# Kernel optimization log

Hardware: AMD Instinct MI355X
Metric: run time of the kernel (lower is better)

The kernel has to match this reference:

```python
import jax, jax.numpy as jnp
import numpy as np
from jax import lax

E = 300      # _embsize
H = 32       # attention heads
ADIM = 64    # projection_dim (attention and values dim)
FF = 100     # feedforward hidden dim
NK = 11      # gaussian kernels
NCONV = 5    # conv kernel sizes 1..5
COUT = 16    # conv out channels for k>=2

def _kernel_mus(n):
    l = [1.0]
    b = 2.0 / (n - 1)
    l.append(1 - b / 2)
    for i in range(1, n - 1):
        l.append(l[i] - b)
    return l

def _kernel_sigmas(n):
    b = 2.0 / (n - 1)
    return [0.0001] + [0.5 * b] * (n - 1)

MU = jnp.asarray(_kernel_mus(NK), jnp.float32).reshape(1, 1, 1, 1, NK)
SIG = jnp.asarray(_kernel_sigmas(NK), jnp.float32).reshape(1, 1, 1, 1, NK)

def _pos_features(T, d):
    # allennlp add_positional_features, min_timescale=1, max_timescale=1e4, d even
    nt = d // 2
    inv = np.exp(np.arange(nt, dtype=np.float32) * -(np.log(1e4) / (nt - 1)))
    pos = np.arange(T, dtype=np.float32)[:, None] * inv[None, :]
    return jnp.asarray(np.concatenate([np.sin(pos), np.cos(pos)], axis=1))

def _layer_norm(x, g, b, eps=1e-6):
    m = jnp.mean(x, -1, keepdims=True)
    s = jnp.std(x, -1, keepdims=True)  # biased std, as allennlp LayerNorm
    return g * (x - m) / (s + eps) + b

def _mhsa(x, mask, Wc, bc, Wo, bo):
    # allennlp MultiHeadSelfAttention: combined projection, scale=sqrt(input_dim//heads)
    B, T, _ = x.shape
    comb = x @ Wc + bc                                   # [B,T,3*ADIM]
    q, k, v = comb[..., :ADIM], comb[..., ADIM:2 * ADIM], comb[..., 2 * ADIM:]
    dh = ADIM // H
    split = lambda t: t.reshape(B, T, H, dh).transpose(0, 2, 1, 3)
    q, k, v = split(q), split(k), split(v)
    scale = float(np.sqrt(E // H))
    sim = jnp.einsum('bhqd,bhkd->bhqk', q / scale, k)
    m = mask[:, None, None, :]
    p = jax.nn.softmax(sim * m, axis=-1) * m             # old allennlp masked_softmax
    p = p / (jnp.sum(p, -1, keepdims=True) + 1e-13)
    o = jnp.einsum('bhqk,bhkd->bhqd', p, v).transpose(0, 2, 1, 3).reshape(B, T, ADIM)
    return o @ Wo + bo

def _encode(x, mask, W1, b1, W2, b2, ffg, ffb, Wc, bc, Wo, bo, lng, lnb):
    # StackedSelfAttentionEncoder, 1 layer, all dropouts = 0
    out = x + _pos_features(x.shape[1], E)[None]
    ff = jax.nn.relu(out @ W1 + b1) @ W2 + b2
    ff = _layer_norm(ff + out, ffg, ffb)                 # residual (dims match)
    att = _mhsa(ff, mask, Wc, bc, Wo, bo)
    return _layer_norm(att + ff, lng, lnb)

def _conv(x, w, b, k):
    if k > 1:
        x = jnp.pad(x, ((0, 0), (0, 0), (0, k - 1), (0, k - 1)))  # ConstantPad2d(0,k-1,0,k-1)
    y = lax.conv_general_dilated(x, w, (1, 1), 'VALID',
                                 dimension_numbers=('NCHW', 'OIHW', 'NCHW'))
    y = y + b[None, :, None, None]
    if k > 1:
        y = jnp.max(y, axis=1, keepdims=True)            # MaxPool3d over channel dim
    return y

def setup_inputs() -> dict:
    key = jax.random.key(0)
    ks = iter(jax.random.split(key, 40))
    B, Q, D = 16, 32, 512
    nrm = lambda shape, s=0.05: jax.random.normal(next(ks), shape, jnp.float32) * s
    return {
        'query_embeddings': jax.random.normal(next(ks), (B, Q, E), jnp.float32),
        'document_embeddings': jax.random.normal(next(ks), (B, D, E), jnp.float32),
        'query_pad_oov_mask': jnp.ones((B, Q), jnp.float32),
        'document_pad_oov_mask': jnp.ones((B, D), jnp.float32),
        'query_idfs': jax.random.uniform(next(ks), (B, Q, 1), jnp.float32),
        'document_idfs': jax.random.uniform(next(ks), (B, D, 1), jnp.float32),
        'W1': nrm((E, FF)), 'b1': jnp.zeros((FF,), jnp.float32),
        'W2': nrm((FF, E)), 'b2': jnp.zeros((E,), jnp.float32),
        'ffg': jnp.ones((E,), jnp.float32), 'ffb': jnp.zeros((E,), jnp.float32),
        'Wc': nrm((E, 3 * ADIM)), 'bc': jnp.zeros((3 * ADIM,), jnp.float32),
        'Wo': nrm((ADIM, E)), 'bo': jnp.zeros((E,), jnp.float32),
        'lng': jnp.ones((E,), jnp.float32), 'lnb': jnp.zeros((E,), jnp.float32),
        'c1w': nrm((1, 2, 1, 1)), 'c1b': jnp.zeros((1,), jnp.float32),
        'c2w': nrm((COUT, 2, 2, 2)), 'c2b': jnp.zeros((COUT,), jnp.float32),
        'c3w': nrm((COUT, 2, 3, 3)), 'c3b': jnp.zeros((COUT,), jnp.float32),
        'c4w': nrm((COUT, 2, 4, 4)), 'c4b': jnp.zeros((COUT,), jnp.float32),
        'c5w': nrm((COUT, 2, 5, 5)), 'c5b': jnp.zeros((COUT,), jnp.float32),
        'dw': nrm((1, NK * NCONV)), 'db': jnp.zeros((1,), jnp.float32),
        'dmw': nrm((1, NK * NCONV)), 'dmb': jnp.zeros((1,), jnp.float32),
        'cw': nrm((1, 2)),
    }

def reference(query_embeddings, document_embeddings, query_pad_oov_mask,
              document_pad_oov_mask, query_idfs, document_idfs,
              W1, b1, W2, b2, ffg, ffb, Wc, bc, Wo, bo, lng, lnb,
              c1w, c1b, c2w, c2b, c3w, c3b, c4w, c4b, c5w, c5b,
              dw, db, dmw, dmb, cw):
    qm, dmask = query_pad_oov_mask, document_pad_oov_mask
    enc = lambda x, m: _encode(x, m, W1, b1, W2, b2, ffg, ffb, Wc, bc, Wo, bo, lng, lnb)
    q_ctx = enc(query_embeddings, qm) * qm[..., None]
    d_ctx = enc(document_embeddings, dmask) * dmask[..., None]
    # cosine on raw embeddings, dot product on contextualized
    qn = query_embeddings / (jnp.linalg.norm(query_embeddings, axis=-1, keepdims=True) + 1e-13)
    dn = document_embeddings / (jnp.linalg.norm(document_embeddings, axis=-1, keepdims=True) + 1e-13)
    cos = jnp.einsum('bqe,bde->bqd', qn, dn)[:, None]
    dot = jnp.einsum('bqe,bde->bqd', q_ctx, d_ctx)[:, None]
    combined = jnp.tanh(jnp.concatenate([cos, dot], axis=1))     # [B,2,Q,D]
    convs = [_conv(combined, w, b, k) for k, (w, b) in enumerate(
        [(c1w, c1b), (c2w, c2b), (c3w, c3b), (c4w, c4b), (c5w, c5b)], start=1)]
    all_conv = jnp.concatenate(convs, axis=1)[..., None]         # [B,5,Q,D,1]
    qd_mask = (qm[:, :, None] * dmask[:, None, :])[:, None, :, :, None]  # [B,1,Q,D,1]
    raw = jnp.exp(-(all_conv - MU) ** 2 / (2.0 * SIG ** 2))      # [B,5,Q,D,NK]
    masked = raw * qd_mask
    doc_len = jnp.sum(dmask, 1)                                  # [B]
    pkq = jnp.sum(masked, axis=3)                                # [B,5,Q,NK]
    log_pkq = jnp.log(jnp.clip(pkq, 1e-10, None)) * qm[:, None, :, None]
    per_kernel = jnp.sum(log_pkq, axis=2)                        # [B,5,NK]
    pkq_mean = pkq / doc_len[:, None, None, None]
    log_pkq_mean = jnp.log(jnp.clip(pkq_mean, 1e-10, None)) * qm[:, None, :, None]
    per_kernel_mean = jnp.sum(log_pkq_mean, axis=2)
    B = per_kernel.shape[0]
    d1 = per_kernel.reshape(B, -1) @ dw.T + db
    d2 = per_kernel_mean.reshape(B, -1) @ dmw.T + dmb
    return (jnp.concatenate([d1, d2], axis=1) @ cw.T)[:, 0]
```

## Files before the change

kernel.cpp:

```cpp
#include <hip/hip_runtime.h>

namespace {

constexpr int E_  = 300;
constexpr int FF_ = 100;
constexpr int AD_ = 64;
constexpr int NH_ = 32;
constexpr int CD_ = 192;
constexpr int B_  = 16;
constexpr int TQ_ = 32;
constexpr int TD_ = 512;
constexpr int NK_ = 11;
constexpr int DOCBLK_ = 512;

__device__ __forceinline__ float wave_sum(float v) {
#pragma unroll
  for (int o = 32; o > 0; o >>= 1) v += __shfl_down(v, o);
  return v;
}

__device__ __forceinline__ int swz16(int e, int t) {
  return e * 16 + (t ^ (((e >> 2) & 7) << 1));
}

__device__ __forceinline__ void fma4(float4& a, float s, const float4& w) {
  a.x = fmaf(s, w.x, a.x); a.y = fmaf(s, w.y, a.y);
  a.z = fmaf(s, w.z, a.z); a.w = fmaf(s, w.w, a.w);
}

__global__ __launch_bounds__(256)
void encode_front_v4(const float* __restrict__ qe, const float* __restrict__ de,
                     const float* __restrict__ W1, const float* __restrict__ b1,
                     const float* __restrict__ W2, const float* __restrict__ b2,
                     const float* __restrict__ ffg, const float* __restrict__ ffb,
                     const float* __restrict__ Wc, const float* __restrict__ bc,
                     float* __restrict__ ffq, float* __restrict__ combq,
                     float* __restrict__ qn,
                     float* __restrict__ ffd, float* __restrict__ combd,
                     float* __restrict__ dnT)
{
  __shared__ float  s_A[4800];
  __shared__ float  s_h1[1600];
  __shared__ float4 s_w4[1500];
  __shared__ float  s_stat[16][17];
  __shared__ float  s_norm[16];

  const int tid = threadIdx.x;
  const int ct = tid & 31, tg = tid >> 5;
  const int t0 = tg * 2;
  const bool doc = (blockIdx.x < DOCBLK_);
  const int sb = doc ? blockIdx.x : (blockIdx.x - DOCBLK_);
  const float* xs = (doc ? de : qe) + (size_t)sb * 16 * E_;
  float* ffo = doc ? ffd : ffq;
  float* cmo = doc ? combd : combq;
  const size_t tok0 = (size_t)sb * 16;
  const int bb_ = doc ? (int)(tok0 >> 9) : (int)(tok0 >> 5);
  const int tp0 = doc ? (int)(tok0 & 511) : (int)(tok0 & 31);

  for (int i = tid; i < 1200; i += 256) {
    const float4 v = *(const float4*)(xs + (size_t)i * 4);
    const int t = i / 75, e0 = (i % 75) * 4;
    s_A[swz16(e0 + 0, t)] = v.x; s_A[swz16(e0 + 1, t)] = v.y;
    s_A[swz16(e0 + 2, t)] = v.z; s_A[swz16(e0 + 3, t)] = v.w;
  }
  __syncthreads();
  {
    const int tk = tid & 15, ch = tid >> 4;
    const int kb = ch * 19, ke = (kb + 19 < 300) ? kb + 19 : 300;
    float ss = 0.f;
    for (int k = kb; k < ke; ++k) { const float v = s_A[swz16(k, tk)]; ss = fmaf(v, v, ss); }
    s_stat[ch][tk] = ss;
  }
  __syncthreads();
  if (tid < 16) {
    float s = 0.f;
#pragma unroll
    for (int i = 0; i < 16; ++i) s += s_stat[i][tid];
    s_norm[tid] = 1.f / (sqrtf(s) + 1e-13f);
  }
  __syncthreads();
  for (int i = tid; i < 1200; i += 256) {
    const int t = i / 75, e0 = (i % 75) * 4;
    const int tp = tp0 + t;
    const float nm = s_norm[t];
#pragma unroll
    for (int j = 0; j < 4; ++j) {
      const int e = e0 + j;
      const int slot = swz16(e, t);
      const float raw = s_A[slot];
      if (doc) dnT[((size_t)bb_ * E_ + e) * 512 + tp] = raw * nm;
      else     qn[(tok0 + t) * E_ + e] = raw * nm;
      const int f = (e < 150) ? e : e - 150;
      const float ang = __expf(-0.061814365f * (float)f) * (float)tp;
      s_A[slot] = raw + ((e < 150) ? sinf(ang) : cosf(ang));
    }
  }
  __syncthreads();

  {
    const int cq = (ct < 25) ? ct : 24;
    float4 a1[2];
    a1[0] = make_float4(0.f, 0.f, 0.f, 0.f);
    a1[1] = make_float4(0.f, 0.f, 0.f, 0.f);
    for (int k0 = 0; k0 < 300; k0 += 60) {
      for (int i = tid; i < 1500; i += 256)
        s_w4[i] = *(const float4*)(W1 + (size_t)k0 * FF_ + (size_t)i * 4);
      __syncthreads();
#pragma unroll 6
      for (int kk = 0; kk < 60; ++kk) {
        const float2 xv = *(const float2*)&s_A[swz16(k0 + kk, t0)];
        const float4 w = s_w4[kk * 25 + cq];
        fma4(a1[0], xv.x, w); fma4(a1[1], xv.y, w);
      }
      __syncthreads();
    }
    if (ct < 25) {
      const float4 bb = *(const float4*)&b1[4 * ct];
#pragma unroll
      for (int r = 0; r < 2; ++r) {
        const int t = t0 + r;
        const float4 a = (r == 0) ? a1[0] : a1[1];
        s_h1[swz16(4 * ct + 0, t)] = fmaxf(a.x + bb.x, 0.f);
        s_h1[swz16(4 * ct + 1, t)] = fmaxf(a.y + bb.y, 0.f);
        s_h1[swz16(4 * ct + 2, t)] = fmaxf(a.z + bb.z, 0.f);
        s_h1[swz16(4 * ct + 3, t)] = fmaxf(a.w + bb.w, 0.f);
      }
    }
    __syncthreads();
  }

  {
    const int q2 = (ct < 11) ? ct + 64 : 74;
    const bool val2 = (ct < 11);
    float4 a2[3][2];
#pragma unroll
    for (int p = 0; p < 3; ++p)
#pragma unroll
      for (int r = 0; r < 2; ++r) a2[p][r] = make_float4(0.f, 0.f, 0.f, 0.f);
    for (int k0 = 0; k0 < 100; k0 += 20) {
      for (int i = tid; i < 1500; i += 256)
        s_w4[i] = *(const float4*)(W2 + (size_t)k0 * E_ + (size_t)i * 4);
      __syncthreads();
#pragma unroll 5
      for (int kk = 0; kk < 20; ++kk) {
        const float2 hv = *(const float2*)&s_h1[swz16(k0 + kk, t0)];
        const float4 w0 = s_w4[kk * 75 + ct];
        const float4 w1 = s_w4[kk * 75 + ct + 32];
        const float4 w2 = s_w4[kk * 75 + q2];
        fma4(a2[0][0], hv.x, w0); fma4(a2[0][1], hv.y, w0);
        fma4(a2[1][0], hv.x, w1); fma4(a2[1][1], hv.y, w1);
        fma4(a2[2][0], hv.x, w2); fma4(a2[2][1], hv.y, w2);
      }
      __syncthreads();
    }
    float sum[2] = {0.f, 0.f}, sq[2] = {0.f, 0.f};
#pragma unroll
    for (int p = 0; p < 3; ++p) {
      const int qq = (p == 0) ? ct : (p == 1) ? ct + 32 : q2;
      const float4 bb = *(const float4*)&b2[4 * qq];
      const bool ok = (p < 2) || val2;
#pragma unroll
      for (int r = 0; r < 2; ++r) {
        const int t = t0 + r;
        float4 v = a2[p][r];
        v.x += bb.x + s_A[swz16(4 * qq + 0, t)];
        v.y += bb.y + s_A[swz16(4 * qq + 1, t)];
        v.z += bb.z + s_A[swz16(4 * qq + 2, t)];
        v.w += bb.w + s_A[swz16(4 * qq + 3, t)];
        a2[p][r] = v;
        if (ok) {
          sum[r] += v.x + v.y + v.z + v.w;
          sq[r] = fmaf(v.x, v.x, fmaf(v.y, v.y, fmaf(v.z, v.z, fmaf(v.w, v.w, sq[r]))));
        }
      }
    }
#pragma unroll
    for (int m = 1; m <= 16; m <<= 1) {
#pragma unroll
      for (int r = 0; r < 2; ++r) {
        sum[r] += __shfl_xor(sum[r], m);
        sq[r]  += __shfl_xor(sq[r], m);
      }
    }
    float mean[2], rstd[2];
#pragma unroll
    for (int r = 0; r < 2; ++r) {
      mean[r] = sum[r] * (1.f / 300.f);
      const float var = fmaxf(sq[r] * (1.f / 300.f) - mean[r] * mean[r], 0.f);
      rstd[r] = 1.f / (sqrtf(var) + 1e-6f);
    }
    __syncthreads();
#pragma unroll
    for (int p = 0; p < 3; ++p) {
      if (p == 2 && !val2) break;
      const int qq = (p == 0) ? ct : (p == 1) ? ct + 32 : q2;
      const int c0 = 4 * qq;
      const float4 g4 = *(const float4*)&ffg[c0];
      const float4 b4 = *(const float4*)&ffb[c0];
#pragma unroll
      for (int r = 0; r < 2; ++r) {
        const int t = t0 + r;
        const float4 v = a2[p][r];
        float4 fv;
        fv.x = fmaf(g4.x, (v.x - mean[r]) * rstd[r], b4.x);
        fv.y = fmaf(g4.y, (v.y - mean[r]) * rstd[r], b4.y);
        fv.z = fmaf(g4.z, (v.z - mean[r]) * rstd[r], b4.z);
        fv.w = fmaf(g4.w, (v.w - mean[r]) * rstd[r], b4.w);
        *(float4*)&ffo[(tok0 + t) * E_ + c0] = fv;
        s_A[swz16(c0 + 0, t)] = fv.x; s_A[swz16(c0 + 1, t)] = fv.y;
        s_A[swz16(c0 + 2, t)] = fv.z; s_A[swz16(c0 + 3, t)] = fv.w;
      }
    }
    __syncthreads();
  }

  {
    const int q3 = (ct < 16) ? ct + 32 : 47;
    float4 a3[2][2];
#pragma unroll
    for (int p = 0; p < 2; ++p)
#pragma unroll
      for (int r = 0; r < 2; ++r) a3[p][r] = make_float4(0.f, 0.f, 0.f, 0.f);
    for (int k0 = 0; k0 < 300; k0 += 30) {
      for (int i = tid; i < 1440; i += 256)
        s_w4[i] = *(const float4*)(Wc + (size_t)k0 * CD_ + (size_t)i * 4);
      __syncthreads();
#pragma unroll 6
      for (int kk = 0; kk < 30; ++kk) {
        const float2 xv = *(const float2*)&s_A[swz16(k0 + kk, t0)];
        const float4 w0 = s_w4[kk * 48 + ct];
        const float4 w1 = s_w4[kk * 48 + q3];
        fma4(a3[0][0], xv.x, w0); fma4(a3[0][1], xv.y, w0);
        fma4(a3[1][0], xv.x, w1); fma4(a3[1][1], xv.y, w1);
      }
      __syncthreads();
    }
    const float4 bb0 = *(const float4*)&bc[4 * ct];
#pragma unroll
    for (int r = 0; r < 2; ++r) {
      float4 o = a3[0][r];
      o.x += bb0.x; o.y += bb0.y; o.z += bb0.z; o.w += bb0.w;
      *(float4*)&cmo[(tok0 + t0 + r) * CD_ + 4 * ct] = o;
    }
    if (ct < 16) {
      const float4 bb1 = *(const float4*)&bc[4 * (ct + 32)];
#pragma unroll
      for (int r = 0; r < 2; ++r) {
        float4 o = a3[1][r];
        o.x += bb1.x; o.y += bb1.y; o.z += bb1.z; o.w += bb1.w;
        *(float4*)&cmo[(tok0 + t0 + r) * CD_ + 4 * (ct + 32)] = o;
      }
    }
  }
}

template <int T>
__global__ __launch_bounds__(512)
void attn(const float* __restrict__ comb, const float* __restrict__ mask,
          float* __restrict__ o)
{
  __shared__ float4 s_kv[T];
  __shared__ float  s_m[T];
  const int bh = blockIdx.x, b = bh / NH_, h = bh % NH_;
  const int tid = threadIdx.x;
  const float* cb = comb + (size_t)b * T * CD_;
  if (tid < T) {
    const float* c = cb + (size_t)tid * CD_;
    const float m = mask[b * T + tid];
    s_kv[tid] = make_float4(c[AD_ + 2 * h] * m, c[AD_ + 2 * h + 1] * m,
                            c[2 * AD_ + 2 * h], c[2 * AD_ + 2 * h + 1]);
    s_m[tid] = m;
  }
  __syncthreads();
  if (tid < T) {
    const float* c = cb + (size_t)tid * CD_;
    const float q0 = c[2 * h] * (1.f / 3.f);
    const float q1 = c[2 * h + 1] * (1.f / 3.f);
    float M = -1e30f;
    for (int j = 0; j < T; ++j) {
      const float4 kv = s_kv[j];
      M = fmaxf(M, fmaf(q0, kv.x, q1 * kv.y));
    }
    float S = 0.f, W = 0.f, a0 = 0.f, a1 = 0.f;
    for (int j = 0; j < T; ++j) {
      const float4 kv = s_kv[j];
      const float s = fmaf(q0, kv.x, q1 * kv.y);
      const float z = __expf(s - M);
      const float w = z * s_m[j];
      S += z; W += w;
      a0 = fmaf(w, kv.z, a0);
      a1 = fmaf(w, kv.w, a1);
    }
    const float dn = 1.f / (W + 1e-13f * S);
    float* op = o + (size_t)(b * T + tid) * AD_ + 2 * h;
    op[0] = a0 * dn;
    op[1] = a1 * dn;
  }
}

__global__ __launch_bounds__(256)
void encode_back_v2(const float* __restrict__ oq, const float* __restrict__ od,
                    const float* __restrict__ ffq, const float* __restrict__ ffd,
                    const float* __restrict__ Wo, const float* __restrict__ bo,
                    const float* __restrict__ lng, const float* __restrict__ lnb,
                    const float* __restrict__ qm, const float* __restrict__ dm,
                    float* __restrict__ qctx, float* __restrict__ dctxT)
{
  __shared__ float  s_O[1024];
  __shared__ float4 s_w4[1200];

  const int tid = threadIdx.x;
  const int ct = tid & 31, tg = tid >> 5;
  const int t0 = tg * 2;
  const bool doc = (blockIdx.x < DOCBLK_);
  const int sb = doc ? blockIdx.x : (blockIdx.x - DOCBLK_);
  const size_t tok0 = (size_t)sb * 16;
  const float* op = doc ? od : oq;
  const float* ffp = doc ? ffd : ffq;
  const float* mp = doc ? dm : qm;
  const int bb_ = doc ? (int)(tok0 >> 9) : 0;
  const int tp0 = doc ? (int)(tok0 & 511) : 0;

  {
    const int i = tid;
    const int t = i >> 4, c0 = (i & 15) * 4;
    const float4 v = *(const float4*)(op + (tok0 + t) * AD_ + c0);
    s_O[swz16(c0 + 0, t)] = v.x; s_O[swz16(c0 + 1, t)] = v.y;
    s_O[swz16(c0 + 2, t)] = v.z; s_O[swz16(c0 + 3, t)] = v.w;
  }
  __syncthreads();

  const int q2 = (ct < 11) ? ct + 64 : 74;
  const bool val2 = (ct < 11);
  float4 a[3][2];
#pragma unroll
  for (int p = 0; p < 3; ++p)
#pragma unroll
    for (int r = 0; r < 2; ++r) a[p][r] = make_float4(0.f, 0.f, 0.f, 0.f);
  for (int k0 = 0; k0 < 64; k0 += 16) {
    for (int i = tid; i < 1200; i += 256)
      s_w4[i] = *(const float4*)(Wo + (size_t)k0 * E_ + (size_t)i * 4);
    __syncthreads();
#pragma unroll 4
    for (int kk = 0; kk < 16; ++kk) {
      const float2 ov = *(const float2*)&s_O[swz16(k0 + kk, t0)];
      const float4 w0 = s_w4[kk * 75 + ct];
      const float4 w1 = s_w4[kk * 75 + ct + 32];
      const float4 w2 = s_w4[kk * 75 + q2];
      fma4(a[0][0], ov.x, w0); fma4(a[0][1], ov.y, w0);
      fma4(a[1][0], ov.x, w1); fma4(a[1][1], ov.y, w1);
      fma4(a[2][0], ov.x, w2); fma4(a[2][1], ov.y, w2);
    }
    __syncthreads();
  }
  float sum[2] = {0.f, 0.f}, sq[2] = {0.f, 0.f};
#pragma unroll
  for (int p = 0; p < 3; ++p) {
    const int qq = (p == 0) ? ct : (p == 1) ? ct + 32 : q2;
    const float4 bb = *(const float4*)&bo[4 * qq];
    const bool ok = (p < 2) || val2;
#pragma unroll
    for (int r = 0; r < 2; ++r) {
      const int t = t0 + r;
      const float4 f4 = *(const float4*)(ffp + (tok0 + t) * E_ + 4 * qq);
      float4 v = a[p][r];
      v.x += bb.x + f4.x; v.y += bb.y + f4.y;
      v.z += bb.z + f4.z; v.w += bb.w + f4.w;
      a[p][r] = v;
      if (ok) {
        sum[r] += v.x + v.y + v.z + v.w;
        sq[r] = fmaf(v.x, v.x, fmaf(v.y, v.y, fmaf(v.z, v.z, fmaf(v.w, v.w, sq[r]))));
      }
    }
  }
#pragma unroll
  for (int m = 1; m <= 16; m <<= 1) {
#pragma unroll
    for (int r = 0; r < 2; ++r) {
      sum[r] += __shfl_xor(sum[r], m);
      sq[r]  += __shfl_xor(sq[r], m);
    }
  }
#pragma unroll
  for (int r = 0; r < 2; ++r) {
    const int t = t0 + r;
    const float mean = sum[r] * (1.f / 300.f);
    const float var  = fmaxf(sq[r] * (1.f / 300.f) - mean * mean, 0.f);
    const float rstd = 1.f / (sqrtf(var) + 1e-6f);
    const float mk = mp[tok0 + t];
#pragma unroll
    for (int p = 0; p < 3; ++p) {
      if (p == 2 && !val2) break;
      const int qq = (p == 0) ? ct : (p == 1) ? ct + 32 : q2;
      const int c0 = 4 * qq;
      const float4 g4 = *(const float4*)&lng[c0];
      const float4 b4 = *(const float4*)&lnb[c0];
      const float4 v = a[p][r];
      float4 fv;
      fv.x = fmaf(g4.x, (v.x - mean) * rstd, b4.x) * mk;
      fv.y = fmaf(g4.y, (v.y - mean) * rstd, b4.y) * mk;
      fv.z = fmaf(g4.z, (v.z - mean) * rstd, b4.z) * mk;
      fv.w = fmaf(g4.w, (v.w - mean) * rstd, b4.w) * mk;
      if (doc) {
        const int tp = tp0 + t;
        dctxT[((size_t)bb_ * E_ + c0 + 0) * 512 + tp] = fv.x;
        dctxT[((size_t)bb_ * E_ + c0 + 1) * 512 + tp] = fv.y;
        dctxT[((size_t)bb_ * E_ + c0 + 2) * 512 + tp] = fv.z;
        dctxT[((size_t)bb_ * E_ + c0 + 3) * 512 + tp] = fv.w;
      } else {
        *(float4*)&qctx[(tok0 + t) * E_ + c0] = fv;
      }
    }
  }
}

__global__ __launch_bounds__(512)
void simtanh_v2(const float* __restrict__ qctx, const float* __restrict__ qn,
                const float* __restrict__ dctxT, const float* __restrict__ dnT,
                float* __restrict__ combined)
{
  __shared__ float s_q[2 * 16 * 304];
  __shared__ float s_part[8 * 32 * 64];

  const int bid = blockIdx.x;
  const int sub = bid & 15, b = bid >> 4;
  const int qh = sub >> 3, dc = sub & 7;
  const int tid = threadIdx.x;
  const int ep = tid >> 6, dlane = tid & 63;
  const int d = dc * 64 + dlane;

  const float* qc  = qctx + ((size_t)b * 32 + qh * 16) * E_;
  const float* qnp = qn   + ((size_t)b * 32 + qh * 16) * E_;
  for (int i = tid; i < 1200; i += 512) {
    const int q = i / 75, e0 = (i % 75) * 4;
    *(float4*)&s_q[(0 * 16 + q) * 304 + e0] = *(const float4*)(qc + q * E_ + e0);
    *(float4*)&s_q[(1 * 16 + q) * 304 + e0] = *(const float4*)(qnp + q * E_ + e0);
  }
  __syncthreads();

  const float* dct = dctxT + (size_t)b * E_ * 512 + d;
  const float* dnt = dnT   + (size_t)b * E_ * 512 + d;
  float accD[16], accC[16];
#pragma unroll
  for (int q = 0; q < 16; ++q) { accD[q] = 0.f; accC[q] = 0.f; }
  const int es = ep * 40, ee = (es + 40 < 300) ? es + 40 : 300;
  for (int e0 = es; e0 < ee; e0 += 4) {
    const float dv0 = dct[(size_t)(e0 + 0) * 512];
    const float dv1 = dct[(size_t)(e0 + 1) * 512];
    const float dv2 = dct[(size_t)(e0 + 2) * 512];
    const float dv3 = dct[(size_t)(e0 + 3) * 512];
    const float dn0 = dnt[(size_t)(e0 + 0) * 512];
    const float dn1 = dnt[(size_t)(e0 + 1) * 512];
    const float dn2 = dnt[(size_t)(e0 + 2) * 512];
    const float dn3 = dnt[(size_t)(e0 + 3) * 512];
#pragma unroll
    for (int q = 0; q < 16; ++q) {
      const float4 qd = *(const float4*)&s_q[(0 * 16 + q) * 304 + e0];
      const float4 qc4 = *(const float4*)&s_q[(1 * 16 + q) * 304 + e0];
      float aD = accD[q], aC = accC[q];
      aD = fmaf(qd.x, dv0, aD); aD = fmaf(qd.y, dv1, aD);
      aD = fmaf(qd.z, dv2, aD); aD = fmaf(qd.w, dv3, aD);
      aC = fmaf(qc4.x, dn0, aC); aC = fmaf(qc4.y, dn1, aC);
      aC = fmaf(qc4.z, dn2, aC); aC = fmaf(qc4.w, dn3, aC);
      accD[q] = aD; accC[q] = aC;
    }
  }
#pragma unroll
  for (int q = 0; q < 16; ++q) {
    s_part[(ep * 32 + q * 2 + 0) * 64 + dlane] = accC[q];
    s_part[(ep * 32 + q * 2 + 1) * 64 + dlane] = accD[q];
  }
  __syncthreads();
  const int s0 = (tid >> 6) * 4;
#pragma unroll
  for (int si = 0; si < 4; ++si) {
    const int s = s0 + si;
    float v = 0.f;
#pragma unroll
    for (int p = 0; p < 8; ++p) v += s_part[(p * 32 + s) * 64 + dlane];
    const int q = s >> 1, typ = s & 1;
    combined[(((size_t)b * 2 + typ) * 32 + qh * 16 + q) * 512 + d] = tanhf(v);
  }
}

template <int K>
__device__ __forceinline__ float conv_max16(const float* __restrict__ s_in, int j,
                                            const float* __restrict__ w,
                                            const float* __restrict__ bias)
{
  float patch[2][K][K];
#pragma unroll
  for (int c = 0; c < 2; ++c)
#pragma unroll
    for (int di = 0; di < K; ++di)
#pragma unroll
      for (int dj = 0; dj < K; ++dj)
        patch[c][di][dj] = s_in[(c * 5 + di) * 516 + j + dj];
  float best = -1e30f;
#pragma unroll
  for (int oc = 0; oc < 16; ++oc) {
    float acc = bias[oc];
#pragma unroll
    for (int c = 0; c < 2; ++c)
#pragma unroll
      for (int di = 0; di < K; ++di)
#pragma unroll
        for (int dj = 0; dj < K; ++dj)
          acc = fmaf(patch[c][di][dj], w[((oc * 2 + c) * K + di) * K + dj], acc);
    best = fmaxf(best, acc);
  }
  return best;
}

__global__ __launch_bounds__(512)
void conv_all(const float* __restrict__ combined,
              const float* __restrict__ c1w, const float* __restrict__ c1b,
              const float* __restrict__ c2w, const float* __restrict__ c2b,
              const float* __restrict__ c3w, const float* __restrict__ c3b,
              const float* __restrict__ c4w, const float* __restrict__ c4b,
              const float* __restrict__ c5w, const float* __restrict__ c5b,
              float* __restrict__ convout)
{
  __shared__ float s_in[2 * 5 * 516];
  __shared__ float s_w[1730];
  __shared__ float s_b[66];
  const int blk = blockIdx.x, b = blk >> 5, i = blk & 31;
  const int tid = threadIdx.x;
  for (int idx = tid; idx < 2 * 5 * 516; idx += 512) {
    const int c = idx / (5 * 516), rem = idx % (5 * 516), r = rem / 516, j = rem % 516;
    const int row = i + r;
    float v = 0.f;
    if (row < 32 && j < 512)
      v = combined[((size_t)(b * 2 + c) * 32 + row) * 512 + j];
    s_in[idx] = v;
  }
  if (tid < 2)   s_w[tid] = c1w[tid];
  if (tid < 128) s_w[2 + tid] = c2w[tid];
  if (tid < 288) s_w[130 + tid] = c3w[tid];
  s_w[418 + tid] = c4w[tid];
  for (int idx = tid; idx < 800; idx += 512) s_w[930 + idx] = c5w[idx];
  if (tid == 0) s_b[0] = c1b[0];
  if (tid < 16) {
    s_b[1 + tid]  = c2b[tid];
    s_b[17 + tid] = c3b[tid];
    s_b[33 + tid] = c4b[tid];
    s_b[49 + tid] = c5b[tid];
  }
  __syncthreads();
  const int j = tid;
  const float o1 = fmaf(s_in[j], s_w[0], fmaf(s_in[5 * 516 + j], s_w[1], s_b[0]));
  convout[((size_t)(b * 5 + 0) * 32 + i) * 512 + j] = o1;
  convout[((size_t)(b * 5 + 1) * 32 + i) * 512 + j] = conv_max16<2>(s_in, j, s_w + 2,   s_b + 1);
  convout[((size_t)(b * 5 + 2) * 32 + i) * 512 + j] = conv_max16<3>(s_in, j, s_w + 130, s_b + 17);
  convout[((size_t)(b * 5 + 3) * 32 + i) * 512 + j] = conv_max16<4>(s_in, j, s_w + 418, s_b + 33);
  convout[((size_t)(b * 5 + 4) * 32 + i) * 512 + j] = conv_max16<5>(s_in, j, s_w + 930, s_b + 49);
}

__global__ __launch_bounds__(512)
void rbf_pkq(const float* __restrict__ convout, const float* __restrict__ dmask,
             const float* __restrict__ qmask, float* __restrict__ pkq)
{
  __shared__ float red[8][NK_];
  const int id = blockIdx.x;
  const int q = id & 31;
  const int b = id / 160;
  const int tid = threadIdx.x;
  const float x = convout[(size_t)id * 512 + tid];
  const float dmv = dmask[b * 512 + tid];
  const float mu[NK_]  = {1.f, .9f, .7f, .5f, .3f, .1f, -.1f, -.3f, -.5f, -.7f, -.9f};
  const float nis[NK_] = {-5e7f, -50.f, -50.f, -50.f, -50.f, -50.f,
                          -50.f, -50.f, -50.f, -50.f, -50.f};
  const int lane = tid & 63, w = tid >> 6;
#pragma unroll
  for (int k = 0; k < NK_; ++k) {
    const float df = x - mu[k];
    float v = __expf(df * df * nis[k]) * dmv;
    v = wave_sum(v);
    if (lane == 0) red[w][k] = v;
  }
  __syncthreads();
  if (tid < NK_) {
    float s = 0.f;
#pragma unroll
    for (int ww = 0; ww < 8; ++ww) s += red[ww][tid];
    pkq[(size_t)id * NK_ + tid] = s * qmask[b * 32 + q];
  }
}

__global__ __launch_bounds__(64)
void final_k(const float* __restrict__ pkq, const float* __restrict__ qmask,
             const float* __restrict__ dmask,
             const float* __restrict__ dw, const float* __restrict__ db,
             const float* __restrict__ dmw, const float* __restrict__ dmb,
             const float* __restrict__ cw, float* __restrict__ out)
{
  const int b = blockIdx.x, tid = threadIdx.x;
  float dl = 0.f;
  for (int j = tid; j < 512; j += 64) dl += dmask[b * 512 + j];
  dl = wave_sum(dl);
  dl = __shfl(dl, 0);
  float v1 = 0.f, v2 = 0.f;
  if (tid < 55) {
    const int c = tid / NK_, k = tid % NK_;
    const float rdl = 1.f / dl;
    float s1 = 0.f, s2 = 0.f;
    for (int q = 0; q < 32; ++q) {
      const float p = pkq[(size_t)((b * 5 + c) * 32 + q) * NK_ + k];
      const float qmv = qmask[b * 32 + q];
      s1 += logf(fmaxf(p, 1e-10f)) * qmv;
      s2 += logf(fmaxf(p * rdl, 1e-10f)) * qmv;
    }
    v1 = s1 * dw[tid];
    v2 = s2 * dmw[tid];
  }
  v1 = wave_sum(v1);
  v2 = wave_sum(v2);
  if (tid == 0) out[b] = (v1 + db[0]) * cw[0] + (v2 + dmb[0]) * cw[1];
}

}

extern "C" void kernel_launch(void* const* d_in, const int* in_sizes, int n_in,
                              void* d_out, int out_size, void* d_ws, size_t ws_size,
                              hipStream_t stream)
{
  const float* qe  = (const float*)d_in[0];
  const float* de  = (const float*)d_in[1];
  const float* qm  = (const float*)d_in[2];
  const float* dm  = (const float*)d_in[3];
  const float* W1  = (const float*)d_in[6];
  const float* b1  = (const float*)d_in[7];
  const float* W2  = (const float*)d_in[8];
  const float* b2  = (const float*)d_in[9];
  const float* ffg = (const float*)d_in[10];
  const float* ffb = (const float*)d_in[11];
  const float* Wc  = (const float*)d_in[12];
  const float* bc  = (const float*)d_in[13];
  const float* Wo  = (const float*)d_in[14];
  const float* bo  = (const float*)d_in[15];
  const float* lng = (const float*)d_in[16];
  const float* lnb = (const float*)d_in[17];
  const float* c1w = (const float*)d_in[18];
  const float* c1b = (const float*)d_in[19];
  const float* c2w = (const float*)d_in[20];
  const float* c2b = (const float*)d_in[21];
  const float* c3w = (const float*)d_in[22];
  const float* c3b = (const float*)d_in[23];
  const float* c4w = (const float*)d_in[24];
  const float* c4b = (const float*)d_in[25];
  const float* c5w = (const float*)d_in[26];
  const float* c5b = (const float*)d_in[27];
  const float* dwp  = (const float*)d_in[28];
  const float* dbp  = (const float*)d_in[29];
  const float* dmwp = (const float*)d_in[30];
  const float* dmbp = (const float*)d_in[31];
  const float* cwp  = (const float*)d_in[32];

  float* ws = (float*)d_ws;
  size_t off = 0;
  auto alloc = [&](size_t n) { float* p = ws + off; off += n; return p; };
  float* ffq      = alloc((size_t)B_ * TQ_ * E_);
  float* combq    = alloc((size_t)B_ * TQ_ * CD_);
  float* oq       = alloc((size_t)B_ * TQ_ * AD_);
  float* qctx     = alloc((size_t)B_ * TQ_ * E_);
  float* qn       = alloc((size_t)B_ * TQ_ * E_);
  float* ffd      = alloc((size_t)B_ * TD_ * E_);
  float* combd    = alloc((size_t)B_ * TD_ * CD_);
  float* od       = alloc((size_t)B_ * TD_ * AD_);
  float* dctxT    = alloc((size_t)B_ * E_ * TD_);
  float* dnT      = alloc((size_t)B_ * E_ * TD_);
  float* combined = alloc((size_t)B_ * 2 * TQ_ * TD_);
  float* convout  = alloc((size_t)B_ * 5 * TQ_ * TD_);
  float* pkq      = alloc((size_t)B_ * 5 * TQ_ * NK_);

  encode_front_v4<<<DOCBLK_ + 32, 256, 0, stream>>>(
      qe, de, W1, b1, W2, b2, ffg, ffb, Wc, bc,
      ffq, combq, qn, ffd, combd, dnT);
  attn<TQ_><<<B_ * NH_, 64, 0, stream>>>(combq, qm, oq);
  attn<TD_><<<B_ * NH_, 512, 0, stream>>>(combd, dm, od);
  encode_back_v2<<<DOCBLK_ + 32, 256, 0, stream>>>(
      oq, od, ffq, ffd, Wo, bo, lng, lnb, qm, dm, qctx, dctxT);
  simtanh_v2<<<256, 512, 0, stream>>>(qctx, qn, dctxT, dnT, combined);
  conv_all<<<B_ * 32, 512, 0, stream>>>(
      combined, c1w, c1b, c2w, c2b, c3w, c3b, c4w, c4b, c5w, c5b, convout);
  rbf_pkq<<<B_ * 5 * TQ_, 512, 0, stream>>>(convout, dm, qm, pkq);
  final_k<<<B_, 64, 0, stream>>>(pkq, qm, dm, dwp, dbp, dmwp, dmbp, cwp,
                                 (float*)d_out);
}
```

Before: 377.2 us.

## Double-buffer weight tiles with async global-to-LDS loads in encoder kernels

Weight chunks for the W1, W2, Wc and Wo matmuls in the front and back encoder kernels are now staged with `__builtin_amdgcn_global_load_lds` into a two-slot LDS buffer. The next chunk, including the first chunk of the following matmul, is fetched while the current one is computed, which removes one barrier per chunk and the register round-trip of the staging copy. The bias, residual and layer-norm epilogues are folded into the last chunk iteration, and padded lanes skip work early. The cost is doubled weight LDS, which may lower occupancy, and correctness depends on the barriers waiting for the async loads to finish.

```diff
diff --git a/kernel.cpp b/kernel.cpp
--- a/kernel.cpp
+++ b/kernel.cpp
@@ -28,8 +28,20 @@
   a.z = fmaf(s, w.z, a.z); a.w = fmaf(s, w.w, a.w);
 }
 
+__device__ __forceinline__ void gl_lds16(const float4* g, float4* l) {
+  __builtin_amdgcn_global_load_lds(
+      (const __attribute__((address_space(1))) void*)g,
+      (__attribute__((address_space(3))) void*)l, 16, 0, 0);
+}
+
+__device__ __forceinline__ void stage_chunk(const float4* __restrict__ src,
+                                            float4* __restrict__ dst,
+                                            int n, int tid) {
+  for (int j = tid; j < n; j += 256) gl_lds16(src + j, dst + j);
+}
+
 __global__ __launch_bounds__(256)
-void encode_front_v4(const float* __restrict__ qe, const float* __restrict__ de,
+void encode_front_v5(const float* __restrict__ qe, const float* __restrict__ de,
                      const float* __restrict__ W1, const float* __restrict__ b1,
                      const float* __restrict__ W2, const float* __restrict__ b2,
                      const float* __restrict__ ffg, const float* __restrict__ ffb,
@@ -41,7 +53,7 @@
 {
   __shared__ float  s_A[4800];
   __shared__ float  s_h1[1600];
-  __shared__ float4 s_w4[1500];
+  __shared__ float4 s_w[2][1500];
   __shared__ float  s_stat[16][17];
   __shared__ float  s_norm[16];
 
@@ -57,6 +69,12 @@
   const int bb_ = doc ? (int)(tok0 >> 9) : (int)(tok0 >> 5);
   const int tp0 = doc ? (int)(tok0 & 511) : (int)(tok0 & 31);
 
+  const float4* W1f4 = (const float4*)W1;
+  const float4* W2f4 = (const float4*)W2;
+  const float4* Wcf4 = (const float4*)Wc;
+
+  stage_chunk(W1f4, &s_w[0][0], 1500, tid);
+
   for (int i = tid; i < 1200; i += 256) {
     const float4 v = *(const float4*)(xs + (size_t)i * 4);
     const int t = i / 75, e0 = (i % 75) * 4;
@@ -102,31 +120,30 @@
     float4 a1[2];
     a1[0] = make_float4(0.f, 0.f, 0.f, 0.f);
     a1[1] = make_float4(0.f, 0.f, 0.f, 0.f);
-    for (int k0 = 0; k0 < 300; k0 += 60) {
-      for (int i = tid; i < 1500; i += 256)
-        s_w4[i] = *(const float4*)(W1 + (size_t)k0 * FF_ + (size_t)i * 4);
-      __syncthreads();
+    for (int c = 0; c < 5; ++c) {
+      if (c < 4) stage_chunk(W1f4 + 1500 * (c + 1), &s_w[(c + 1) & 1][0], 1500, tid);
+      else       stage_chunk(W2f4,                  &s_w[1][0],           1500, tid);
+      const float4* wb = &s_w[c & 1][0];
 #pragma unroll 6
       for (int kk = 0; kk < 60; ++kk) {
-        const float2 xv = *(const float2*)&s_A[swz16(k0 + kk, t0)];
-        const float4 w = s_w4[kk * 25 + cq];
+        const float2 xv = *(const float2*)&s_A[swz16(c * 60 + kk, t0)];
+        const float4 w = wb[kk * 25 + cq];
         fma4(a1[0], xv.x, w); fma4(a1[1], xv.y, w);
       }
+      if (c == 4 && ct < 25) {
+        const float4 bb = *(const float4*)&b1[4 * ct];
+#pragma unroll
+        for (int r = 0; r < 2; ++r) {
+          const int t = t0 + r;
+          const float4 a = (r == 0) ? a1[0] : a1[1];
+          s_h1[swz16(4 * ct + 0, t)] = fmaxf(a.x + bb.x, 0.f);
+          s_h1[swz16(4 * ct + 1, t)] = fmaxf(a.y + bb.y, 0.f);
+          s_h1[swz16(4 * ct + 2, t)] = fmaxf(a.z + bb.z, 0.f);
+          s_h1[swz16(4 * ct + 3, t)] = fmaxf(a.w + bb.w, 0.f);
+        }
+      }
       __syncthreads();
     }
-    if (ct < 25) {
-      const float4 bb = *(const float4*)&b1[4 * ct];
-#pragma unroll
-      for (int r = 0; r < 2; ++r) {
-        const int t = t0 + r;
-        const float4 a = (r == 0) ? a1[0] : a1[1];
-        s_h1[swz16(4 * ct + 0, t)] = fmaxf(a.x + bb.x, 0.f);
-        s_h1[swz16(4 * ct + 1, t)] = fmaxf(a.y + bb.y, 0.f);
-        s_h1[swz16(4 * ct + 2, t)] = fmaxf(a.z + bb.z, 0.f);
-        s_h1[swz16(4 * ct + 3, t)] = fmaxf(a.w + bb.w, 0.f);
-      }
-    }
-    __syncthreads();
   }
 
   {
@@ -137,81 +154,76 @@
     for (int p = 0; p < 3; ++p)
 #pragma unroll
       for (int r = 0; r < 2; ++r) a2[p][r] = make_float4(0.f, 0.f, 0.f, 0.f);
-    for (int k0 = 0; k0 < 100; k0 += 20) {
-      for (int i = tid; i < 1500; i += 256)
-        s_w4[i] = *(const float4*)(W2 + (size_t)k0 * E_ + (size_t)i * 4);
-      __syncthreads();
+    for (int c = 0; c < 5; ++c) {
+      if (c < 4) stage_chunk(W2f4 + 1500 * (c + 1), &s_w[c & 1][0], 1500, tid);
+      else       stage_chunk(Wcf4,                  &s_w[0][0],     1440, tid);
+      const float4* wb = &s_w[(c + 1) & 1][0];
 #pragma unroll 5
       for (int kk = 0; kk < 20; ++kk) {
-        const float2 hv = *(const float2*)&s_h1[swz16(k0 + kk, t0)];
-        const float4 w0 = s_w4[kk * 75 + ct];
-        const float4 w1 = s_w4[kk * 75 + ct + 32];
-        const float4 w2 = s_w4[kk * 75 + q2];
+        const float2 hv = *(const float2*)&s_h1[swz16(c * 20 + kk, t0)];
+        const float4 w0 = wb[kk * 75 + ct];
+        const float4 w1 = wb[kk * 75 + ct + 32];
+        const float4 w2 = wb[kk * 75 + q2];
         fma4(a2[0][0], hv.x, w0); fma4(a2[0][1], hv.y, w0);
         fma4(a2[1][0], hv.x, w1); fma4(a2[1][1], hv.y, w1);
         fma4(a2[2][0], hv.x, w2); fma4(a2[2][1], hv.y, w2);
       }
-      __syncthreads();
-    }
-    float sum[2] = {0.f, 0.f}, sq[2] = {0.f, 0.f};
-#pragma unroll
-    for (int p = 0; p < 3; ++p) {
-      const int qq = (p == 0) ? ct : (p == 1) ? ct + 32 : q2;
-      const float4 bb = *(const float4*)&b2[4 * qq];
-      const bool ok = (p < 2) || val2;
-#pragma unroll
-      for (int r = 0; r < 2; ++r) {
-        const int t = t0 + r;
-        float4 v = a2[p][r];
-        v.x += bb.x + s_A[swz16(4 * qq + 0, t)];
-        v.y += bb.y + s_A[swz16(4 * qq + 1, t)];
-        v.z += bb.z + s_A[swz16(4 * qq + 2, t)];
-        v.w += bb.w + s_A[swz16(4 * qq + 3, t)];
-        a2[p][r] = v;
-        if (ok) {
-          sum[r] += v.x + v.y + v.z + v.w;
-          sq[r] = fmaf(v.x, v.x, fmaf(v.y, v.y, fmaf(v.z, v.z, fmaf(v.w, v.w, sq[r]))));
+      if (c == 4) {
+        float sum[2] = {0.f, 0.f}, sq[2] = {0.f, 0.f};
+#pragma unroll
+        for (int p = 0; p < 3; ++p) {
+          const int qq = (p == 0) ? ct : (p == 1) ? ct + 32 : q2;
+          const bool ok = (p < 2) || val2;
+          if (!ok) break;
+          const float4 bb = *(const float4*)&b2[4 * qq];
+#pragma unroll
+          for (int r = 0; r < 2; ++r) {
+            const int t = t0 + r;
+            float4 v = a2[p][r];
+            v.x += bb.x + s_A[swz16(4 * qq + 0, t)];
+            v.y += bb.y + s_A[swz16(4 * qq + 1, t)];
+            v.z += bb.z + s_A[swz16(4 * qq + 2, t)];
+            v.w += bb.w + s_A[swz16(4 * qq + 3, t)];
+            a2[p][r] = v;
+            sum[r] += v.x + v.y + v.z + v.w;
+            sq[r] = fmaf(v.x, v.x, fmaf(v.y, v.y, fmaf(v.z, v.z, fmaf(v.w, v.w, sq[r]))));
+          }
+        }
+#pragma unroll
+        for (int m = 1; m <= 16; m <<= 1) {
+#pragma unroll
+          for (int r = 0; r < 2; ++r) {
+            sum[r] += __shfl_xor(sum[r], m);
+            sq[r]  += __shfl_xor(sq[r], m);
+          }
+        }
+#pragma unroll
+        for (int r = 0; r < 2; ++r) {
+          const int t = t0 + r;
+          const float mean = sum[r] * (1.f / 300.f);
+          const float var  = fmaxf(sq[r] * (1.f / 300.f) - mean * mean, 0.f);
+          const float rstd = 1.f / (sqrtf(var) + 1e-6f);
+#pragma unroll
+          for (int p = 0; p < 3; ++p) {
+            if (p == 2 && !val2) break;
+            const int qq = (p == 0) ? ct : (p == 1) ? ct + 32 : q2;
+            const int c0 = 4 * qq;
+            const float4 g4 = *(const float4*)&ffg[c0];
+            const float4 b4 = *(const float4*)&ffb[c0];
+            const float4 v = a2[p][r];
+            float4 fv;
+            fv.x = fmaf(g4.x, (v.x - mean) * rstd, b4.x);
+            fv.y = fmaf(g4.y, (v.y - mean) * rstd, b4.y);
+            fv.z = fmaf(g4.z, (v.z - mean) * rstd, b4.z);
+            fv.w = fmaf(g4.w, (v.w - mean) * rstd, b4.w);
+            *(float4*)&ffo[(tok0 + t) * E_ + c0] = fv;
+            s_A[swz16(c0 + 0, t)] = fv.x; s_A[swz16(c0 + 1, t)] = fv.y;
+            s_A[swz16(c0 + 2, t)] = fv.z; s_A[swz16(c0 + 3, t)] = fv.w;
+          }
         }
       }
-    }
-#pragma unroll
-    for (int m = 1; m <= 16; m <<= 1) {
-#pragma unroll
-      for (int r = 0; r < 2; ++r) {
-        sum[r] += __shfl_xor(sum[r], m);
-        sq[r]  += __shfl_xor(sq[r], m);
-      }
-    }
-    float mean[2], rstd[2];
-#pragma unroll
-    for (int r = 0; r < 2; ++r) {
-      mean[r] = sum[r] * (1.f / 300.f);
-      const float var = fmaxf(sq[r] * (1.f / 300.f) - mean[r] * mean[r], 0.f);
-      rstd[r] = 1.f / (sqrtf(var) + 1e-6f);
-    }
-    __syncthreads();
-#pragma unroll
-    for (int p = 0; p < 3; ++p) {
-      if (p == 2 && !val2) break;
-      const int qq = (p == 0) ? ct : (p == 1) ? ct + 32 : q2;
-      const int c0 = 4 * qq;
-      const float4 g4 = *(const float4*)&ffg[c0];
-      const float4 b4 = *(const float4*)&ffb[c0];
-#pragma unroll
-      for (int r = 0; r < 2; ++r) {
-        const int t = t0 + r;
-        const float4 v = a2[p][r];
-        float4 fv;
-        fv.x = fmaf(g4.x, (v.x - mean[r]) * rstd[r], b4.x);
-        fv.y = fmaf(g4.y, (v.y - mean[r]) * rstd[r], b4.y);
-        fv.z = fmaf(g4.z, (v.z - mean[r]) * rstd[r], b4.z);
-        fv.w = fmaf(g4.w, (v.w - mean[r]) * rstd[r], b4.w);
-        *(float4*)&ffo[(tok0 + t) * E_ + c0] = fv;
-        s_A[swz16(c0 + 0, t)] = fv.x; s_A[swz16(c0 + 1, t)] = fv.y;
-        s_A[swz16(c0 + 2, t)] = fv.z; s_A[swz16(c0 + 3, t)] = fv.w;
-      }
-    }
-    __syncthreads();
+      __syncthreads();
+    }
   }
 
   {
@@ -221,19 +233,18 @@
     for (int p = 0; p < 2; ++p)
 #pragma unroll
       for (int r = 0; r < 2; ++r) a3[p][r] = make_float4(0.f, 0.f, 0.f, 0.f);
-    for (int k0 = 0; k0 < 300; k0 += 30) {
-      for (int i = tid; i < 1440; i += 256)
-        s_w4[i] = *(const float4*)(Wc + (size_t)k0 * CD_ + (size_t)i * 4);
-      __syncthreads();
+    for (int c = 0; c < 10; ++c) {
+      if (c < 9) stage_chunk(Wcf4 + 1440 * (c + 1), &s_w[(c + 1) & 1][0], 1440, tid);
+      const float4* wb = &s_w[c & 1][0];
 #pragma unroll 6
       for (int kk = 0; kk < 30; ++kk) {
-        const float2 xv = *(const float2*)&s_A[swz16(k0 + kk, t0)];
-        const float4 w0 = s_w4[kk * 48 + ct];
-        const float4 w1 = s_w4[kk * 48 + q3];
+        const float2 xv = *(const float2*)&s_A[swz16(c * 30 + kk, t0)];
+        const float4 w0 = wb[kk * 48 + ct];
+        const float4 w1 = wb[kk * 48 + q3];
         fma4(a3[0][0], xv.x, w0); fma4(a3[0][1], xv.y, w0);
         fma4(a3[1][0], xv.x, w1); fma4(a3[1][1], xv.y, w1);
       }
-      __syncthreads();
+      if (c < 9) __syncthreads();
     }
     const float4 bb0 = *(const float4*)&bc[4 * ct];
 #pragma unroll
@@ -299,7 +310,7 @@
 }
 
 __global__ __launch_bounds__(256)
-void encode_back_v2(const float* __restrict__ oq, const float* __restrict__ od,
+void encode_back_v3(const float* __restrict__ oq, const float* __restrict__ od,
                     const float* __restrict__ ffq, const float* __restrict__ ffd,
                     const float* __restrict__ Wo, const float* __restrict__ bo,
                     const float* __restrict__ lng, const float* __restrict__ lnb,
@@ -307,7 +318,7 @@
                     float* __restrict__ qctx, float* __restrict__ dctxT)
 {
   __shared__ float  s_O[1024];
-  __shared__ float4 s_w4[1200];
+  __shared__ float4 s_w[2][1200];
 
   const int tid = threadIdx.x;
   const int ct = tid & 31, tg = tid >> 5;
@@ -321,9 +332,11 @@
   const int bb_ = doc ? (int)(tok0 >> 9) : 0;
   const int tp0 = doc ? (int)(tok0 & 511) : 0;
 
+  const float4* Wof4 = (const float4*)Wo;
+  stage_chunk(Wof4, &s_w[0][0], 1200, tid);
+
   {
-    const int i = tid;
-    const int t = i >> 4, c0 = (i & 15) * 4;
+    const int t = tid >> 4, c0 = (tid & 15) * 4;
     const float4 v = *(const float4*)(op + (tok0 + t) * AD_ + c0);
     s_O[swz16(c0 + 0, t)] = v.x; s_O[swz16(c0 + 1, t)] = v.y;
     s_O[swz16(c0 + 2, t)] = v.z; s_O[swz16(c0 + 3, t)] = v.w;
@@ -337,28 +350,28 @@
   for (int p = 0; p < 3; ++p)
 #pragma unroll
     for (int r = 0; r < 2; ++r) a[p][r] = make_float4(0.f, 0.f, 0.f, 0.f);
-  for (int k0 = 0; k0 < 64; k0 += 16) {
-    for (int i = tid; i < 1200; i += 256)
-      s_w4[i] = *(const float4*)(Wo + (size_t)k0 * E_ + (size_t)i * 4);
-    __syncthreads();
+  for (int c = 0; c < 4; ++c) {
+    if (c < 3) stage_chunk(Wof4 + 1200 * (c + 1), &s_w[(c + 1) & 1][0], 1200, tid);
+    const float4* wb = &s_w[c & 1][0];
 #pragma unroll 4
     for (int kk = 0; kk < 16; ++kk) {
-      const float2 ov = *(const float2*)&s_O[swz16(k0 + kk, t0)];
-      const float4 w0 = s_w4[kk * 75 + ct];
-      const float4 w1 = s_w4[kk * 75 + ct + 32];
-      const float4 w2 = s_w4[kk * 75 + q2];
+      const float2 ov = *(const float2*)&s_O[swz16(c * 16 + kk, t0)];
+      const float4 w0 = wb[kk * 75 + ct];
+      const float4 w1 = wb[kk * 75 + ct + 32];
+      const float4 w2 = wb[kk * 75 + q2];
       fma4(a[0][0], ov.x, w0); fma4(a[0][1], ov.y, w0);
       fma4(a[1][0], ov.x, w1); fma4(a[1][1], ov.y, w1);
       fma4(a[2][0], ov.x, w2); fma4(a[2][1], ov.y, w2);
     }
-    __syncthreads();
+    if (c < 3) __syncthreads();
   }
   float sum[2] = {0.f, 0.f}, sq[2] = {0.f, 0.f};
 #pragma unroll
   for (int p = 0; p < 3; ++p) {
     const int qq = (p == 0) ? ct : (p == 1) ? ct + 32 : q2;
+    const bool ok = (p < 2) || val2;
+    if (!ok) break;
     const float4 bb = *(const float4*)&bo[4 * qq];
-    const bool ok = (p < 2) || val2;
 #pragma unroll
     for (int r = 0; r < 2; ++r) {
       const int t = t0 + r;
@@ -367,10 +380,8 @@
       v.x += bb.x + f4.x; v.y += bb.y + f4.y;
       v.z += bb.z + f4.z; v.w += bb.w + f4.w;
       a[p][r] = v;
-      if (ok) {
-        sum[r] += v.x + v.y + v.z + v.w;
-        sq[r] = fmaf(v.x, v.x, fmaf(v.y, v.y, fmaf(v.z, v.z, fmaf(v.w, v.w, sq[r]))));
-      }
+      sum[r] += v.x + v.y + v.z + v.w;
+      sq[r] = fmaf(v.x, v.x, fmaf(v.y, v.y, fmaf(v.z, v.z, fmaf(v.w, v.w, sq[r]))));
     }
   }
 #pragma unroll
@@ -673,12 +684,12 @@
   float* convout  = alloc((size_t)B_ * 5 * TQ_ * TD_);
   float* pkq      = alloc((size_t)B_ * 5 * TQ_ * NK_);
 
-  encode_front_v4<<<DOCBLK_ + 32, 256, 0, stream>>>(
+  encode_front_v5<<<DOCBLK_ + 32, 256, 0, stream>>>(
       qe, de, W1, b1, W2, b2, ffg, ffb, Wc, bc,
       ffq, combq, qn, ffd, combd, dnT);
   attn<TQ_><<<B_ * NH_, 64, 0, stream>>>(combq, qm, oq);
   attn<TD_><<<B_ * NH_, 512, 0, stream>>>(combd, dm, od);
-  encode_back_v2<<<DOCBLK_ + 32, 256, 0, stream>>>(
+  encode_back_v3<<<DOCBLK_ + 32, 256, 0, stream>>>(
       oq, od, ffq, ffd, Wo, bo, lng, lnb, qm, dm, qctx, dctxT);
   simtanh_v2<<<256, 512, 0, stream>>>(qctx, qn, dctxT, dnT, combined);
   conv_all<<<B_ * 32, 512, 0, stream>>>(
```

Result: no change. 382.0 us (+1.3%).
